# Kernel tuning notes

Measured on AMD Instinct MI355X. Metric: run time of the kernel, lower is better.

The kernel has to match this reference:

```python
import jax, jax.numpy as jnp
import numpy as np

# ---- static configuration (matches init_kwargs / input_specs) ----
B, N = 4, 128            # images, proposals per image
C = 256                  # feature channels (in_channels)
HF, WF = 23, 30          # feature map size (input 736x960 / 32)
PH, PW = 7, 7            # pooled_size
SCALE = 1.0 / 32.0       # scale_factor
HIMG, WIMG = HF * 32, WF * 32
KH = HF // PH + 2        # max rows any pooling bin can span
KW = WF // PW + 2        # max cols any pooling bin can span
HID, OUT = 256, 5
NEG = -1e30


def _roi_pool_one(f, box):
    """Quantized ROI max pooling for one proposal.
    f: (C, HF, WF) feature map; box: (4,) [x1,y1,x2,y2] in feature coords.
    Returns (C, PH, PW)."""
    box = jax.lax.stop_gradient(box)  # indices are non-differentiable
    x1 = jnp.clip(jnp.floor(box[0]).astype(jnp.int32), 0, WF - 1)
    y1 = jnp.clip(jnp.floor(box[1]).astype(jnp.int32), 0, HF - 1)
    roi_w = jnp.clip(jnp.ceil(box[2]).astype(jnp.int32) - x1, 1, WF)
    roi_h = jnp.clip(jnp.ceil(box[3]).astype(jnp.int32) - y1, 1, HF)
    ph = jnp.arange(PH)
    pw = jnp.arange(PW)
    hs = y1 + (ph * roi_h) // PH                       # bin row starts (PH,)
    he = y1 + ((ph + 1) * roi_h + PH - 1) // PH        # bin row ends (ceil)
    ws = x1 + (pw * roi_w) // PW
    we = x1 + ((pw + 1) * roi_w + PW - 1) // PW
    hidx = hs[:, None] + jnp.arange(KH)[None, :]       # (PH, KH)
    hval = (hidx < he[:, None]) & (hidx < HF)
    widx = ws[:, None] + jnp.arange(KW)[None, :]       # (PW, KW)
    wval = (widx < we[:, None]) & (widx < WF)
    rows = f[:, jnp.clip(hidx, 0, HF - 1), :]          # (C, PH, KH, WF) gather
    rmax = jnp.max(jnp.where(hval[None, :, :, None], rows, NEG), axis=2)  # (C, PH, WF)
    cols = rmax[:, :, jnp.clip(widx, 0, WF - 1)]       # (C, PH, PW, KW) gather
    return jnp.max(jnp.where(wval[None, None], cols, NEG), axis=3)        # (C, PH, PW)


# vmap over proposals, then over images: (B,C,HF,WF),(B,N,4) -> (B,N,C,PH,PW)
_roi_pool = jax.vmap(jax.vmap(_roi_pool_one, in_axes=(None, 0)), in_axes=(0, 0))


def setup_inputs() -> dict:
    key = jax.random.key(0)
    ks = jax.random.split(key, 8)
    features = jax.random.normal(ks[0], (B, C, HF, WF), jnp.float32)
    # valid proposals in image coordinates (min box side ~32 px)
    x1 = jax.random.uniform(ks[1], (B, N)) * (WIMG - 32.0)
    y1 = jax.random.uniform(ks[2], (B, N)) * (HIMG - 32.0)
    x2 = x1 + 32.0 + jax.random.uniform(ks[3], (B, N)) * (WIMG - 32.0 - x1)
    y2 = y1 + 32.0 + jax.random.uniform(ks[4], (B, N)) * (HIMG - 32.0 - y1)
    conf = jax.random.normal(ks[5], (B, N))
    proposals = jnp.stack([x1, y1, x2, y2, conf], axis=-1)  # (B, N, 5)
    W1 = jax.random.normal(ks[6], (HID, C * PH * PW), jnp.float32) * 0.01
    b1 = jnp.zeros((HID,), jnp.float32)
    W2 = jax.random.normal(ks[7], (OUT, HID), jnp.float32) * 0.01
    b2 = jnp.zeros((OUT,), jnp.float32)
    return {"features": features, "proposals": proposals,
            "W1": W1, "b1": b1, "W2": W2, "b2": b2}


def reference(features, proposals, W1, b1, W2, b2):
    boxes_feat = proposals[..., :4] * SCALE                 # image -> feature coords
    pooled = _roi_pool(features, boxes_feat)                # (B, N, C, PH, PW)
    flat = pooled.reshape(B, N, C * PH * PW)
    h = jax.nn.relu(jnp.einsum('bnf,hf->bnh', flat, W1) + b1)
    out = jnp.einsum('bnh,oh->bno', h, W2) + b2             # (B, N, 5)
    refined_boxes = proposals[..., :4] + out[..., :4]
    refined_conf = jax.nn.sigmoid(proposals[..., 4:5] + out[..., 4:5])
    return jnp.concatenate([refined_boxes, refined_conf], axis=-1)  # (B, N, 5)
```

## Files before the change

kernel.cpp:

```cpp
#include <hip/hip_runtime.h>
#include <math.h>

#define Bq 4
#define Nq 128
#define Cq 256
#define HFq 23
#define WFq 30
#define PHq 7
#define PWq 7
#define HIDq 256
#define OUTq 5
#define Fq (Cq*PHq*PWq)
#define Mq (Bq*Nq)
#define HWq (HFq*WFq)
#define SCALEq (1.0f/32.0f)
#define NEGq (-1e30f)
#define KHq 5
#define KWq 6
#define SPLITK 56
#define KCH (Fq/SPLITK)
#define KSTEPS (KCH/32)
#define TJOBS 704

typedef float f32x4 __attribute__((ext_vector_type(4)));
typedef __bf16 bf16x8 __attribute__((ext_vector_type(8)));

__device__ __forceinline__ unsigned short f2b(float f) {
    unsigned int u = __float_as_uint(f);
    unsigned int r = (u + 0x7FFFu + ((u >> 16) & 1u)) >> 16;
    return (unsigned short)r;
}
__device__ __forceinline__ float b2f(unsigned short s) {
    return __uint_as_float(((unsigned int)s) << 16);
}

union PrepSM {
    float t[32][33];
    unsigned short s[Fq];
};

__global__ __launch_bounds__(256) void k_prep(const float* __restrict__ feat,
                                              const float* __restrict__ W1,
                                              unsigned short* __restrict__ ft,
                                              unsigned short* __restrict__ w1p) {
    __shared__ __align__(16) PrepSM sm;
    int tid = threadIdx.x, bid = blockIdx.x;
    if (bid < TJOBS) {
        int bb = bid / 176;
        int rem = bid - bb * 176;
        int cblk = rem / 22;
        int xblk = rem - cblk * 22;
        const float* src = feat + (size_t)bb * Cq * HWq;
        unsigned short* dst = ft + (size_t)bb * HWq * Cq;
        int x0 = xblk * 32, c0 = cblk * 32;
        int tx = tid & 31, ty = tid >> 5;
#pragma unroll
        for (int i = 0; i < 4; ++i) {
            int c = c0 + ty + i * 8, x = x0 + tx;
            if (x < HWq) sm.t[ty + i * 8][tx] = src[(size_t)c * HWq + x];
        }
        __syncthreads();
#pragma unroll
        for (int i = 0; i < 4; ++i) {
            int x = x0 + ty + i * 8, c = c0 + tx;
            if (x < HWq) dst[(size_t)x * Cq + c] = f2b(sm.t[tx][ty + i * 8]);
        }
    } else {
        int j = bid - TJOBS;
        const float4* src = (const float4*)(W1 + (size_t)j * Fq);
        for (int i = tid; i < Fq / 4; i += 256) {
            float4 v = src[i];
            ushort4 o;
            o.x = f2b(v.x); o.y = f2b(v.y); o.z = f2b(v.z); o.w = f2b(v.w);
            ((ushort4*)sm.s)[i] = o;
        }
        __syncthreads();
        uint4* dst = (uint4*)(w1p + (size_t)j * Fq);
        for (int i = tid; i < Fq / 8; i += 256) {
            int base = i * 8;
            int cell = base >> 8;
            int c0 = base & 255;
            unsigned short tmp[8];
#pragma unroll
            for (int u = 0; u < 8; ++u) tmp[u] = sm.s[(c0 + u) * 49 + cell];
            dst[i] = *(const uint4*)tmp;
        }
    }
}

__global__ __launch_bounds__(256) void k_pool(const unsigned short* __restrict__ ft,
                                              const float* __restrict__ props,
                                              unsigned short* __restrict__ pooled) {
    int wave = threadIdx.x >> 6;
    int lane = threadIdx.x & 63;
    int g = blockIdx.y * 4 + wave;
    int m = blockIdx.x;
    int b = m >> 7;
    const float* pr = props + (size_t)m * 5;
    float b0 = pr[0] * SCALEq, b1v = pr[1] * SCALEq;
    float b2v = pr[2] * SCALEq, b3v = pr[3] * SCALEq;
    int x1 = min(max((int)floorf(b0), 0), WFq - 1);
    int y1 = min(max((int)floorf(b1v), 0), HFq - 1);
    int rw = min(max((int)ceilf(b2v) - x1, 1), WFq);
    int rh = min(max((int)ceilf(b3v) - y1, 1), HFq);
    const unsigned short* ftb = ft + (size_t)b * HWq * Cq + lane * 4;
    unsigned short* pm = pooled + (size_t)m * Fq + lane * 4;

    for (int cell = g; cell < PHq * PWq; cell += 8) {
        int ph = cell / 7;
        int pw = cell - ph * 7;
        int hs = y1 + (ph * rh) / PHq;
        int he = min(y1 + ((ph + 1) * rh + PHq - 1) / PHq, HFq);
        int wss = x1 + (pw * rw) / PWq;
        int wee = min(x1 + ((pw + 1) * rw + PWq - 1) / PWq, WFq);
        f32x4 acc = {NEGq, NEGq, NEGq, NEGq};
#pragma unroll
        for (int kh = 0; kh < KHq; ++kh) {
            if (hs + kh < he) {
                const unsigned short* rowp = ftb + (size_t)((hs + kh) * WFq) * Cq;
#pragma unroll
                for (int kw = 0; kw < KWq; ++kw) {
                    if (wss + kw < wee) {
                        ushort4 v = *(const ushort4*)(rowp + (size_t)(wss + kw) * Cq);
                        acc.x = fmaxf(acc.x, b2f(v.x));
                        acc.y = fmaxf(acc.y, b2f(v.y));
                        acc.z = fmaxf(acc.z, b2f(v.z));
                        acc.w = fmaxf(acc.w, b2f(v.w));
                    }
                }
            }
        }
        ushort4 o;
        o.x = f2b(acc.x); o.y = f2b(acc.y); o.z = f2b(acc.z); o.w = f2b(acc.w);
        *(ushort4*)(pm + (size_t)cell * Cq) = o;
    }
}

__global__ __launch_bounds__(256) void k_gemm1(const unsigned short* __restrict__ pooled,
                                               const unsigned short* __restrict__ w1p,
                                               float* __restrict__ part) {
    int tid = threadIdx.x;
    int wv = tid >> 6, lane = tid & 63;
    int q = lane >> 4, mr = lane & 15;
    int m0 = blockIdx.x * 64;
    int j0 = wv * 64;
    int kz = blockIdx.y;

    const uint4* ap[4];
    const uint4* bp[4];
#pragma unroll
    for (int g = 0; g < 4; ++g) {
        ap[g] = (const uint4*)(pooled + (size_t)(m0 + g * 16 + mr) * Fq + kz * KCH + q * 8);
        bp[g] = (const uint4*)(w1p   + (size_t)(j0 + g * 16 + mr) * Fq + kz * KCH + q * 8);
    }

    f32x4 acc[4][4];
#pragma unroll
    for (int a = 0; a < 4; ++a)
#pragma unroll
        for (int b = 0; b < 4; ++b) acc[a][b] = (f32x4){0.f, 0.f, 0.f, 0.f};

    uint4 abuf[3][4], bbuf[3][4];
#pragma unroll
    for (int g = 0; g < 4; ++g) {
        abuf[0][g] = ap[g][0]; bbuf[0][g] = bp[g][0];
        abuf[1][g] = ap[g][4]; bbuf[1][g] = bp[g][4];
    }
#pragma unroll
    for (int s = 0; s < KSTEPS; ++s) {
        int cur = s % 3;
        int nxt = (s + 2) % 3;
        if (s + 2 < KSTEPS) {
#pragma unroll
            for (int g = 0; g < 4; ++g) {
                abuf[nxt][g] = ap[g][(s + 2) * 4];
                bbuf[nxt][g] = bp[g][(s + 2) * 4];
            }
        }
#pragma unroll
        for (int mg = 0; mg < 4; ++mg) {
            bf16x8 af = *(const bf16x8*)&abuf[cur][mg];
#pragma unroll
            for (int jg = 0; jg < 4; ++jg) {
                bf16x8 bf = *(const bf16x8*)&bbuf[cur][jg];
                acc[mg][jg] = __builtin_amdgcn_mfma_f32_16x16x32_bf16(af, bf, acc[mg][jg], 0, 0, 0);
            }
        }
    }
    float* pbase = part + (size_t)kz * Mq * HIDq;
#pragma unroll
    for (int mg = 0; mg < 4; ++mg) {
        int mb = m0 + mg * 16 + q * 4;
#pragma unroll
        for (int jg = 0; jg < 4; ++jg) {
            int jj = j0 + jg * 16 + mr;
#pragma unroll
            for (int r2 = 0; r2 < 4; ++r2) {
                pbase[(size_t)(mb + r2) * HIDq + jj] = acc[mg][jg][r2];
            }
        }
    }
}

__global__ __launch_bounds__(256) void k_tail(const float* __restrict__ part,
                                              const float* __restrict__ b1,
                                              const float* __restrict__ W2,
                                              const float* __restrict__ b2,
                                              const float* __restrict__ props,
                                              float* __restrict__ out) {
    __shared__ float red[OUTq][4];
    int m = blockIdx.x, j = threadIdx.x;
    float s = 0.f;
#pragma unroll
    for (int z = 0; z < SPLITK; ++z) s += part[((size_t)z * Mq + m) * HIDq + j];
    s += b1[j];
    float hv = fmaxf(s, 0.f);
    float p[OUTq];
#pragma unroll
    for (int o = 0; o < OUTq; ++o) p[o] = hv * W2[(size_t)o * HIDq + j];
    int lane = j & 63, wid = j >> 6;
#pragma unroll
    for (int o = 0; o < OUTq; ++o) {
        float v = p[o];
        v += __shfl_xor(v, 1);
        v += __shfl_xor(v, 2);
        v += __shfl_xor(v, 4);
        v += __shfl_xor(v, 8);
        v += __shfl_xor(v, 16);
        v += __shfl_xor(v, 32);
        if (lane == 0) red[o][wid] = v;
    }
    __syncthreads();
    if (j < OUTq) {
        float sv = red[j][0] + red[j][1] + red[j][2] + red[j][3] + b2[j];
        float pv = props[(size_t)m * 5 + j];
        float rr;
        if (j < 4) rr = pv + sv;
        else rr = 1.f / (1.f + expf(-(pv + sv)));
        out[(size_t)m * 5 + j] = rr;
    }
}

extern "C" void kernel_launch(void* const* d_in, const int* in_sizes, int n_in,
                              void* d_out, int out_size, void* d_ws, size_t ws_size,
                              hipStream_t stream) {
    const float* feat  = (const float*)d_in[0];
    const float* props = (const float*)d_in[1];
    const float* W1    = (const float*)d_in[2];
    const float* b1    = (const float*)d_in[3];
    const float* W2    = (const float*)d_in[4];
    const float* b2    = (const float*)d_in[5];
    float* out = (float*)d_out;

    char* ws = (char*)d_ws;
    unsigned short* ft     = (unsigned short*)(ws);
    unsigned short* w1p    = (unsigned short*)(ws + 1413120);
    unsigned short* pooled = (unsigned short*)(ws + 7835648);
    float* part            = (float*)(ws + 20680704);

    k_prep<<<TJOBS + HIDq, 256, 0, stream>>>(feat, W1, ft, w1p);
    k_pool<<<dim3(Mq, 2), 256, 0, stream>>>(ft, props, pooled);
    k_gemm1<<<dim3(8, SPLITK), 256, 0, stream>>>(pooled, w1p, part);
    k_tail<<<Mq, 256, 0, stream>>>(part, b1, W2, b2, props, out);
}
```

Before: 134.8 us.

## Retile GEMM1 with per-block N split and smaller split-K factor

GEMM1 blocks now cover a 64x64 output tile, with each wave computing 16 rows by 64 columns. Previously each block covered 64 rows by the full 256 hidden columns, with each wave owning 64x64. Split-K drops from 56 to 14, so each block works through a longer K chunk, which cuts the partial-sum traffic written to workspace and re-read by the tail kernel. The trade-off is less register-level reuse (one A fragment per wave instead of four), so the same W1 data is loaded more times across blocks. The total grid stays at 448 blocks.

```diff
diff --git a/kernel.cpp b/kernel.cpp
--- a/kernel.cpp
+++ b/kernel.cpp
@@ -17,7 +17,7 @@
 #define NEGq (-1e30f)
 #define KHq 5
 #define KWq 6
-#define SPLITK 56
+#define SPLITK 14
 #define KCH (Fq/SPLITK)
 #define KSTEPS (KCH/32)
 #define TJOBS 704
@@ -143,61 +143,48 @@
     int wv = tid >> 6, lane = tid & 63;
     int q = lane >> 4, mr = lane & 15;
     int m0 = blockIdx.x * 64;
-    int j0 = wv * 64;
-    int kz = blockIdx.y;
-
-    const uint4* ap[4];
+    int j0 = blockIdx.y * 64;
+    int kz = blockIdx.z;
+
+    const uint4* ap = (const uint4*)(pooled + (size_t)(m0 + wv * 16 + mr) * Fq + kz * KCH + q * 8);
     const uint4* bp[4];
 #pragma unroll
-    for (int g = 0; g < 4; ++g) {
-        ap[g] = (const uint4*)(pooled + (size_t)(m0 + g * 16 + mr) * Fq + kz * KCH + q * 8);
-        bp[g] = (const uint4*)(w1p   + (size_t)(j0 + g * 16 + mr) * Fq + kz * KCH + q * 8);
-    }
-
-    f32x4 acc[4][4];
-#pragma unroll
-    for (int a = 0; a < 4; ++a)
-#pragma unroll
-        for (int b = 0; b < 4; ++b) acc[a][b] = (f32x4){0.f, 0.f, 0.f, 0.f};
-
-    uint4 abuf[3][4], bbuf[3][4];
-#pragma unroll
-    for (int g = 0; g < 4; ++g) {
-        abuf[0][g] = ap[g][0]; bbuf[0][g] = bp[g][0];
-        abuf[1][g] = ap[g][4]; bbuf[1][g] = bp[g][4];
-    }
-#pragma unroll
+    for (int g = 0; g < 4; ++g)
+        bp[g] = (const uint4*)(w1p + (size_t)(j0 + g * 16 + mr) * Fq + kz * KCH + q * 8);
+
+    f32x4 acc[4];
+#pragma unroll
+    for (int g = 0; g < 4; ++g) acc[g] = (f32x4){0.f, 0.f, 0.f, 0.f};
+
+    uint4 abuf[3], bbuf[3][4];
+    abuf[0] = ap[0]; abuf[1] = ap[4];
+#pragma unroll
+    for (int g = 0; g < 4; ++g) { bbuf[0][g] = bp[g][0]; bbuf[1][g] = bp[g][4]; }
+
+#pragma unroll 4
     for (int s = 0; s < KSTEPS; ++s) {
         int cur = s % 3;
         int nxt = (s + 2) % 3;
         if (s + 2 < KSTEPS) {
-#pragma unroll
-            for (int g = 0; g < 4; ++g) {
-                abuf[nxt][g] = ap[g][(s + 2) * 4];
-                bbuf[nxt][g] = bp[g][(s + 2) * 4];
-            }
-        }
-#pragma unroll
-        for (int mg = 0; mg < 4; ++mg) {
-            bf16x8 af = *(const bf16x8*)&abuf[cur][mg];
-#pragma unroll
-            for (int jg = 0; jg < 4; ++jg) {
-                bf16x8 bf = *(const bf16x8*)&bbuf[cur][jg];
-                acc[mg][jg] = __builtin_amdgcn_mfma_f32_16x16x32_bf16(af, bf, acc[mg][jg], 0, 0, 0);
-            }
+            abuf[nxt] = ap[(s + 2) * 4];
+#pragma unroll
+            for (int g = 0; g < 4; ++g) bbuf[nxt][g] = bp[g][(s + 2) * 4];
+        }
+        bf16x8 af = *(const bf16x8*)&abuf[cur];
+#pragma unroll
+        for (int jg = 0; jg < 4; ++jg) {
+            bf16x8 bf = *(const bf16x8*)&bbuf[cur][jg];
+            acc[jg] = __builtin_amdgcn_mfma_f32_16x16x32_bf16(af, bf, acc[jg], 0, 0, 0);
         }
     }
     float* pbase = part + (size_t)kz * Mq * HIDq;
-#pragma unroll
-    for (int mg = 0; mg < 4; ++mg) {
-        int mb = m0 + mg * 16 + q * 4;
-#pragma unroll
-        for (int jg = 0; jg < 4; ++jg) {
-            int jj = j0 + jg * 16 + mr;
-#pragma unroll
-            for (int r2 = 0; r2 < 4; ++r2) {
-                pbase[(size_t)(mb + r2) * HIDq + jj] = acc[mg][jg][r2];
-            }
+    int mb = m0 + wv * 16 + q * 4;
+#pragma unroll
+    for (int jg = 0; jg < 4; ++jg) {
+        int jj = j0 + jg * 16 + mr;
+#pragma unroll
+        for (int r2 = 0; r2 < 4; ++r2) {
+            pbase[(size_t)(mb + r2) * HIDq + jj] = acc[jg][r2];
         }
     }
 }
@@ -260,6 +247,6 @@
 
     k_prep<<<TJOBS + HIDq, 256, 0, stream>>>(feat, W1, ft, w1p);
     k_pool<<<dim3(Mq, 2), 256, 0, stream>>>(ft, props, pooled);
-    k_gemm1<<<dim3(8, SPLITK), 256, 0, stream>>>(pooled, w1p, part);
+    k_gemm1<<<dim3(8, 4, SPLITK), 256, 0, stream>>>(pooled, w1p, part);
     k_tail<<<Mq, 256, 0, stream>>>(part, b1, W2, b2, props, out);
 }
```

After: 218.0 us. +61.7%, slower.
